# Kernel optimization log

Hardware: AMD Instinct MI355X
Metric: run time of the kernel (lower is better)

## Reference

```python
import jax, jax.numpy as jnp
import numpy as np

B, M, K, N = 4, 2048, 4096, 4096


def setup_inputs() -> dict:
    key = jax.random.key(0)
    k1, k2, k3, k4, k5 = jax.random.split(key, 5)
    # quantized activations in [-8, 7], stored as int8 (spec dtype int32, cast here)
    x_q = jax.random.randint(k1, (B, M, K), -8, 8, dtype=jnp.int32).astype(jnp.int8)
    # per-token activation scales (B, M, 1)
    scales_x = jax.random.uniform(k2, (B, M, 1), dtype=jnp.float32, minval=0.001, maxval=0.02)
    # int8 weight (N, K) in [-8, 7] as produced by from_float
    weight = jax.random.randint(k3, (N, K), -8, 8, dtype=jnp.int32).astype(jnp.int8)
    # per-output-row weight scales (N, 1)
    weight_scales = jax.random.uniform(k4, (N, 1), dtype=jnp.float32, minval=0.001, maxval=0.02)
    bias = jax.random.normal(k5, (N,), dtype=jnp.float32) * 0.02
    return {"x_q": x_q, "scales_x": scales_x, "weight": weight,
            "weight_scales": weight_scales, "bias": bias}


def reference(x_q, scales_x, weight, weight_scales, bias):
    acc = jnp.einsum('bmk,nk->bmn', x_q, weight,
                     preferred_element_type=jnp.int32)  # (B, M, N) int32
    # sym_dequant: per-token scale * per-row weight scale, then fused bias add
    out = acc.astype(jnp.float32) * scales_x * weight_scales.reshape(1, 1, N) + bias
    return out
```

## Files before the change

### kernel.cpp

```cpp
#include <hip/hip_runtime.h>
#include <stdint.h>

#define MROWS 8192
#define K_DIM 4096
#define N_DIM 4096
#define BM 256
#define BN 256
#define BK 64
#define KT (K_DIM / BK)
#define ABYTES (BM * BK)
#define TBYTES (2 * ABYTES)

#define X_ELEMS (MROWS * K_DIM)
#define W_ELEMS (N_DIM * K_DIM)

typedef __attribute__((ext_vector_type(4))) int   int4v;
typedef __attribute__((ext_vector_type(4))) float float4v;

#define GLOAD_LDS16(gptr, lptr)                                                   \
    __builtin_amdgcn_global_load_lds((const __attribute__((address_space(1))) void*)(gptr), \
                                     (__attribute__((address_space(3))) void*)(lptr), 16, 0, 0)

__device__ __forceinline__ int pack4(int4v v) {
    return (int)((unsigned)(v[0] & 0xFF)
               | ((unsigned)(v[1] & 0xFF) << 8)
               | ((unsigned)(v[2] & 0xFF) << 16)
               | ((unsigned)(v[3] & 0xFF) << 24));
}

__global__ __launch_bounds__(256) void pack_i32_to_i8(
    const int4v* __restrict__ src, int* __restrict__ dst, int n4)
{
    int i = blockIdx.x * blockDim.x + threadIdx.x;
    if (i < n4) dst[i] = pack4(src[i]);
}

__global__ __launch_bounds__(512, 2) void i8gemm_dq_kernel(
    const int8_t* __restrict__ xq,
    const float*  __restrict__ sx,
    const int8_t* __restrict__ wt,
    const float*  __restrict__ ws,
    const float*  __restrict__ bias,
    float*        __restrict__ out)
{
    __shared__ __align__(16) int8_t lds8[4 * TBYTES];

    const int tid  = threadIdx.x;
    const int wave = tid >> 6;
    const int lane = tid & 63;
    const int wr   = wave >> 2;
    const int wcn  = wave & 3;

    const int bid = blockIdx.x;
    const int wg  = (bid & 7) * 64 + (bid >> 3);
    const int ct  = wg & 15;
    const int rt  = wg >> 4;

    const int srow = wave * 16 + (lane >> 2);
    const int scol = (((lane & 3) - ((lane >> 3) & 3)) & 3) * 16;
    const int8_t* gA0 = xq + (size_t)(rt * BM + srow) * K_DIM + scol;
    const int8_t* gA1 = gA0 + (size_t)128 * K_DIM;
    const int8_t* gB0 = wt + (size_t)(ct * BN + srow) * K_DIM + scol;
    const int8_t* gB1 = gB0 + (size_t)128 * K_DIM;
    const int dA0 = wave * 1024;
    const int dA1 = 8192 + wave * 1024;
    const int dB0 = ABYTES + wave * 1024;
    const int dB1 = ABYTES + 8192 + wave * 1024;

    const int mrow = lane & 15;
    const int kswz = (((lane >> 4) + (mrow >> 1)) & 3) * 16;
    const int aoff = (wr * 128 + mrow) * BK + kswz;
    const int boff = ABYTES + (wcn * 64 + mrow) * BK + kswz;

    int4v acc[8][4] = {};

    #pragma unroll
    for (int u = 0; u < 3; ++u) {
        const size_t ko = (size_t)u * BK;
        int8_t* bb = lds8 + u * TBYTES;
        GLOAD_LDS16(gA0 + ko, bb + dA0);
        GLOAD_LDS16(gA1 + ko, bb + dA1);
        GLOAD_LDS16(gB0 + ko, bb + dB0);
        GLOAD_LDS16(gB1 + ko, bb + dB1);
    }

    #pragma unroll 4
    for (int t = 0; t < KT; ++t) {
        const int  buf = t & 3;
        const int  nb  = (t + 3) & 3;
        const int  u   = (t + 3) & (KT - 1);
        const size_t ko = (size_t)u * BK;
        const int8_t* base = lds8 + buf * TBYTES;
        int8_t* nbb = lds8 + nb * TBYTES;

        asm volatile("s_waitcnt vmcnt(8)" ::: "memory");
        __builtin_amdgcn_s_barrier();
        __builtin_amdgcn_sched_barrier(0);

        int4v a[4], b[4];
        #pragma unroll
        for (int i = 0; i < 4; ++i) a[i] = *(const int4v*)(base + aoff + i * 1024);
        #pragma unroll
        for (int j = 0; j < 4; ++j) b[j] = *(const int4v*)(base + boff + j * 1024);
        GLOAD_LDS16(gA0 + ko, nbb + dA0);
        GLOAD_LDS16(gA1 + ko, nbb + dA1);

        __builtin_amdgcn_s_setprio(1);
        #pragma unroll
        for (int i = 0; i < 4; ++i)
            #pragma unroll
            for (int j = 0; j < 4; ++j)
                acc[i][j] = __builtin_amdgcn_mfma_i32_16x16x64_i8(a[i], b[j], acc[i][j], 0, 0, 0);
        __builtin_amdgcn_s_setprio(0);

        int4v a2[4];
        #pragma unroll
        for (int i = 0; i < 4; ++i) a2[i] = *(const int4v*)(base + aoff + (4 + i) * 1024);
        GLOAD_LDS16(gB0 + ko, nbb + dB0);
        GLOAD_LDS16(gB1 + ko, nbb + dB1);

        __builtin_amdgcn_s_setprio(1);
        #pragma unroll
        for (int i = 0; i < 4; ++i)
            #pragma unroll
            for (int j = 0; j < 4; ++j)
                acc[4 + i][j] = __builtin_amdgcn_mfma_i32_16x16x64_i8(a2[i], b[j], acc[4 + i][j], 0, 0, 0);
        __builtin_amdgcn_s_setprio(0);
    }

    asm volatile("s_waitcnt vmcnt(0)" ::: "memory");

    const int row_base = rt * BM + wr * 128;
    const int col_base = ct * BN + wcn * 64;
    const int crow = (lane >> 4) * 4;
    const int ccol = lane & 15;

    float wsc[4], bsc[4];
    #pragma unroll
    for (int j = 0; j < 4; ++j) {
        const int c = col_base + j * 16 + ccol;
        wsc[j] = ws[c];
        bsc[j] = bias[c];
    }

    #pragma unroll
    for (int i = 0; i < 8; ++i) {
        const int r0 = row_base + i * 16 + crow;
        const float4v sx4 = *(const float4v*)(sx + r0);
        #pragma unroll
        for (int j = 0; j < 4; ++j) {
            const int c = col_base + j * 16 + ccol;
            float* o = out + (size_t)r0 * N_DIM + c;
            #pragma unroll
            for (int r = 0; r < 4; ++r)
                o[(size_t)r * N_DIM] = (float)acc[i][j][r] * sx4[r] * wsc[j] + bsc[j];
        }
    }
}

extern "C" void kernel_launch(void* const* d_in, const int* in_sizes, int n_in,
                              void* d_out, int out_size, void* d_ws, size_t ws_size,
                              hipStream_t stream) {
    const int*   xq32 = (const int*)d_in[0];
    const float* sx   = (const float*)d_in[1];
    const int*   wt32 = (const int*)d_in[2];
    const float* ws   = (const float*)d_in[3];
    const float* bias = (const float*)d_in[4];
    float* out = (float*)d_out;

    int8_t* xq8 = (int8_t*)d_ws;
    int8_t* wt8 = xq8 + (size_t)X_ELEMS;

    {
        int n4x = X_ELEMS / 4;
        int n4w = W_ELEMS / 4;
        pack_i32_to_i8<<<n4x / 256, 256, 0, stream>>>((const int4v*)xq32, (int*)xq8, n4x);
        pack_i32_to_i8<<<n4w / 256, 256, 0, stream>>>((const int4v*)wt32, (int*)wt8, n4w);
    }

    dim3 grid((MROWS / BM) * (N_DIM / BN));
    i8gemm_dq_kernel<<<grid, 512, 0, stream>>>(xq8, sx, wt8, ws, bias, out);
}
```

Before: 388.5 us.

## Register double-buffer LDS fragments across K tiles and merge pack kernels

```diff
diff --git a/kernel.cpp b/kernel.cpp
--- a/kernel.cpp
+++ b/kernel.cpp
@@ -29,11 +29,44 @@
 }
 
 __global__ __launch_bounds__(256) void pack_i32_to_i8(
-    const int4v* __restrict__ src, int* __restrict__ dst, int n4)
+    const int4v* __restrict__ srcX, int* __restrict__ dstX, int n4x,
+    const int4v* __restrict__ srcW, int* __restrict__ dstW, int n4w)
 {
-    int i = blockIdx.x * blockDim.x + threadIdx.x;
-    if (i < n4) dst[i] = pack4(src[i]);
+    const int stride = gridDim.x * blockDim.x;
+    const int n4 = n4x + n4w;
+    for (int i = blockIdx.x * blockDim.x + threadIdx.x; i < n4; i += stride) {
+        if (i < n4x) dstX[i] = pack4(srcX[i]);
+        else         dstW[i - n4x] = pack4(srcW[i - n4x]);
+    }
 }
+
+
+#define TILE_BODY(T, AC, BC, AN, BN_)                                          \
+  {                                                                            \
+    asm volatile("s_waitcnt vmcnt(4)" ::: "memory");                           \
+    __builtin_amdgcn_s_barrier();                                              \
+    __builtin_amdgcn_sched_barrier(0);                                         \
+    const int u_ = ((T) + 3) & (KT - 1);                                       \
+    const size_t ko_ = (size_t)u_ * BK;                                        \
+    int8_t* nbb_ = lds8 + (((T) + 3) & 3) * TBYTES;                            \
+    GLOAD_LDS16(gA0 + ko_, nbb_ + dA0);                                        \
+    GLOAD_LDS16(gA1 + ko_, nbb_ + dA1);                                        \
+    GLOAD_LDS16(gB0 + ko_, nbb_ + dB0);                                        \
+    GLOAD_LDS16(gB1 + ko_, nbb_ + dB1);                                        \
+    const int8_t* rb_ = lds8 + (((T) + 1) & 3) * TBYTES;                       \
+    _Pragma("unroll") for (int i_ = 0; i_ < 8; ++i_)                           \
+        AN[i_] = *(const int4v*)(rb_ + aoff + i_ * 1024);                      \
+    _Pragma("unroll") for (int j_ = 0; j_ < 4; ++j_)                           \
+        BN_[j_] = *(const int4v*)(rb_ + boff + j_ * 1024);                     \
+    __builtin_amdgcn_sched_barrier(0);                                         \
+    __builtin_amdgcn_s_setprio(1);                                             \
+    _Pragma("unroll") for (int i_ = 0; i_ < 8; ++i_)                           \
+      _Pragma("unroll") for (int j_ = 0; j_ < 4; ++j_)                         \
+        acc[i_][j_] = __builtin_amdgcn_mfma_i32_16x16x64_i8(                   \
+                          AC[i_], BC[j_], acc[i_][j_], 0, 0, 0);               \
+    __builtin_amdgcn_s_setprio(0);                                             \
+    __builtin_amdgcn_sched_barrier(0);                                         \
+  }
 
 __global__ __launch_bounds__(512, 2) void i8gemm_dq_kernel(
     const int8_t* __restrict__ xq,
@@ -84,48 +117,21 @@
         GLOAD_LDS16(gB1 + ko, bb + dB1);
     }
 
-    #pragma unroll 4
-    for (int t = 0; t < KT; ++t) {
-        const int  buf = t & 3;
-        const int  nb  = (t + 3) & 3;
-        const int  u   = (t + 3) & (KT - 1);
-        const size_t ko = (size_t)u * BK;
-        const int8_t* base = lds8 + buf * TBYTES;
-        int8_t* nbb = lds8 + nb * TBYTES;
-
+    int4v a0f[8], b0f[4], a1f[8], b1f[4];
+    {
         asm volatile("s_waitcnt vmcnt(8)" ::: "memory");
         __builtin_amdgcn_s_barrier();
         __builtin_amdgcn_sched_barrier(0);
+        const int8_t* rb = lds8;
+        #pragma unroll
+        for (int i = 0; i < 8; ++i) a0f[i] = *(const int4v*)(rb + aoff + i * 1024);
+        #pragma unroll
+        for (int j = 0; j < 4; ++j) b0f[j] = *(const int4v*)(rb + boff + j * 1024);
+    }
 
-        int4v a[4], b[4];
-        #pragma unroll
-        for (int i = 0; i < 4; ++i) a[i] = *(const int4v*)(base + aoff + i * 1024);
-        #pragma unroll
-        for (int j = 0; j < 4; ++j) b[j] = *(const int4v*)(base + boff + j * 1024);
-        GLOAD_LDS16(gA0 + ko, nbb + dA0);
-        GLOAD_LDS16(gA1 + ko, nbb + dA1);
-
-        __builtin_amdgcn_s_setprio(1);
-        #pragma unroll
-        for (int i = 0; i < 4; ++i)
-            #pragma unroll
-            for (int j = 0; j < 4; ++j)
-                acc[i][j] = __builtin_amdgcn_mfma_i32_16x16x64_i8(a[i], b[j], acc[i][j], 0, 0, 0);
-        __builtin_amdgcn_s_setprio(0);
-
-        int4v a2[4];
-        #pragma unroll
-        for (int i = 0; i < 4; ++i) a2[i] = *(const int4v*)(base + aoff + (4 + i) * 1024);
-        GLOAD_LDS16(gB0 + ko, nbb + dB0);
-        GLOAD_LDS16(gB1 + ko, nbb + dB1);
-
-        __builtin_amdgcn_s_setprio(1);
-        #pragma unroll
-        for (int i = 0; i < 4; ++i)
-            #pragma unroll
-            for (int j = 0; j < 4; ++j)
-                acc[4 + i][j] = __builtin_amdgcn_mfma_i32_16x16x64_i8(a2[i], b[j], acc[4 + i][j], 0, 0, 0);
-        __builtin_amdgcn_s_setprio(0);
+    for (int tt = 0; tt < KT; tt += 2) {
+        TILE_BODY(tt,     a0f, b0f, a1f, b1f);
+        TILE_BODY(tt + 1, a1f, b1f, a0f, b0f);
     }
 
     asm volatile("s_waitcnt vmcnt(0)" ::: "memory");
@@ -174,8 +180,8 @@
     {
         int n4x = X_ELEMS / 4;
         int n4w = W_ELEMS / 4;
-        pack_i32_to_i8<<<n4x / 256, 256, 0, stream>>>((const int4v*)xq32, (int*)xq8, n4x);
-        pack_i32_to_i8<<<n4w / 256, 256, 0, stream>>>((const int4v*)wt32, (int*)wt8, n4w);
+        pack_i32_to_i8<<<2048, 256, 0, stream>>>((const int4v*)xq32, (int*)xq8, n4x,
+                                                 (const int4v*)wt32, (int*)wt8, n4w);
     }
 
     dim3 grid((MROWS / BM) * (N_DIM / BN));
```

Result: no change. 392.7 us (+1.1%).

## Switch GEMM to 32x32x32 int8 MFMA tiles and merge pack kernels

Applied to the files above, without the earlier changes.

```diff
diff --git a/kernel.cpp b/kernel.cpp
--- a/kernel.cpp
+++ b/kernel.cpp
@@ -14,8 +14,9 @@
 #define X_ELEMS (MROWS * K_DIM)
 #define W_ELEMS (N_DIM * K_DIM)
 
-typedef __attribute__((ext_vector_type(4))) int   int4v;
-typedef __attribute__((ext_vector_type(4))) float float4v;
+typedef __attribute__((ext_vector_type(4)))  int   int4v;
+typedef __attribute__((ext_vector_type(16))) int   int16v;
+typedef __attribute__((ext_vector_type(4)))  float float4v;
 
 #define GLOAD_LDS16(gptr, lptr)                                                   \
     __builtin_amdgcn_global_load_lds((const __attribute__((address_space(1))) void*)(gptr), \
@@ -29,10 +30,15 @@
 }
 
 __global__ __launch_bounds__(256) void pack_i32_to_i8(
-    const int4v* __restrict__ src, int* __restrict__ dst, int n4)
+    const int4v* __restrict__ srcX, int* __restrict__ dstX, int n4x,
+    const int4v* __restrict__ srcW, int* __restrict__ dstW, int n4w)
 {
-    int i = blockIdx.x * blockDim.x + threadIdx.x;
-    if (i < n4) dst[i] = pack4(src[i]);
+    const int stride = gridDim.x * blockDim.x;
+    const int n4 = n4x + n4w;
+    for (int i = blockIdx.x * blockDim.x + threadIdx.x; i < n4; i += stride) {
+        if (i < n4x) dstX[i] = pack4(srcX[i]);
+        else         dstW[i - n4x] = pack4(srcW[i - n4x]);
+    }
 }
 
 __global__ __launch_bounds__(512, 2) void i8gemm_dq_kernel(
@@ -67,12 +73,13 @@
     const int dB0 = ABYTES + wave * 1024;
     const int dB1 = ABYTES + 8192 + wave * 1024;
 
-    const int mrow = lane & 15;
-    const int kswz = (((lane >> 4) + (mrow >> 1)) & 3) * 16;
-    const int aoff = (wr * 128 + mrow) * BK + kswz;
-    const int boff = ABYTES + (wcn * 64 + mrow) * BK + kswz;
-
-    int4v acc[8][4] = {};
+    const int m32 = lane & 31;
+    const int hi  = lane >> 5;
+    const int askew = ((hi + (m32 >> 1)) & 3) * 16;
+    const int aoff  = (wr * 128 + m32) * BK;
+    const int boff  = ABYTES + (wcn * 64 + m32) * BK;
+
+    int16v acc[4][2] = {};
 
     #pragma unroll
     for (int u = 0; u < 3; ++u) {
@@ -97,34 +104,49 @@
         __builtin_amdgcn_s_barrier();
         __builtin_amdgcn_sched_barrier(0);
 
-        int4v a[4], b[4];
-        #pragma unroll
-        for (int i = 0; i < 4; ++i) a[i] = *(const int4v*)(base + aoff + i * 1024);
-        #pragma unroll
-        for (int j = 0; j < 4; ++j) b[j] = *(const int4v*)(base + boff + j * 1024);
+        int4v a0[2][2], bf[2][2];
+        #pragma unroll
+        for (int i = 0; i < 2; ++i)
+            #pragma unroll
+            for (int s = 0; s < 2; ++s)
+                a0[i][s] = *(const int4v*)(base + aoff + i * 2048 + (askew ^ (s << 5)));
+        #pragma unroll
+        for (int j = 0; j < 2; ++j)
+            #pragma unroll
+            for (int s = 0; s < 2; ++s)
+                bf[j][s] = *(const int4v*)(base + boff + j * 2048 + (askew ^ (s << 5)));
         GLOAD_LDS16(gA0 + ko, nbb + dA0);
         GLOAD_LDS16(gA1 + ko, nbb + dA1);
 
         __builtin_amdgcn_s_setprio(1);
         #pragma unroll
-        for (int i = 0; i < 4; ++i)
-            #pragma unroll
-            for (int j = 0; j < 4; ++j)
-                acc[i][j] = __builtin_amdgcn_mfma_i32_16x16x64_i8(a[i], b[j], acc[i][j], 0, 0, 0);
+        for (int s = 0; s < 2; ++s)
+            #pragma unroll
+            for (int i = 0; i < 2; ++i)
+                #pragma unroll
+                for (int j = 0; j < 2; ++j)
+                    acc[i][j] = __builtin_amdgcn_mfma_i32_32x32x32_i8(
+                                    a0[i][s], bf[j][s], acc[i][j], 0, 0, 0);
         __builtin_amdgcn_s_setprio(0);
 
-        int4v a2[4];
-        #pragma unroll
-        for (int i = 0; i < 4; ++i) a2[i] = *(const int4v*)(base + aoff + (4 + i) * 1024);
+        int4v a1[2][2];
+        #pragma unroll
+        for (int i = 0; i < 2; ++i)
+            #pragma unroll
+            for (int s = 0; s < 2; ++s)
+                a1[i][s] = *(const int4v*)(base + aoff + (2 + i) * 2048 + (askew ^ (s << 5)));
         GLOAD_LDS16(gB0 + ko, nbb + dB0);
         GLOAD_LDS16(gB1 + ko, nbb + dB1);
 
         __builtin_amdgcn_s_setprio(1);
         #pragma unroll
-        for (int i = 0; i < 4; ++i)
-            #pragma unroll
-            for (int j = 0; j < 4; ++j)
-                acc[4 + i][j] = __builtin_amdgcn_mfma_i32_16x16x64_i8(a2[i], b[j], acc[4 + i][j], 0, 0, 0);
+        for (int s = 0; s < 2; ++s)
+            #pragma unroll
+            for (int i = 0; i < 2; ++i)
+                #pragma unroll
+                for (int j = 0; j < 2; ++j)
+                    acc[2 + i][j] = __builtin_amdgcn_mfma_i32_32x32x32_i8(
+                                        a1[i][s], bf[j][s], acc[2 + i][j], 0, 0, 0);
         __builtin_amdgcn_s_setprio(0);
     }
 
@@ -132,28 +154,29 @@
 
     const int row_base = rt * BM + wr * 128;
     const int col_base = ct * BN + wcn * 64;
-    const int crow = (lane >> 4) * 4;
-    const int ccol = lane & 15;
-
-    float wsc[4], bsc[4];
+
+    float wsc[2], bsc[2];
     #pragma unroll
-    for (int j = 0; j < 4; ++j) {
-        const int c = col_base + j * 16 + ccol;
+    for (int j = 0; j < 2; ++j) {
+        const int c = col_base + j * 32 + m32;
         wsc[j] = ws[c];
         bsc[j] = bias[c];
     }
 
     #pragma unroll
-    for (int i = 0; i < 8; ++i) {
-        const int r0 = row_base + i * 16 + crow;
-        const float4v sx4 = *(const float4v*)(sx + r0);
-        #pragma unroll
-        for (int j = 0; j < 4; ++j) {
-            const int c = col_base + j * 16 + ccol;
-            float* o = out + (size_t)r0 * N_DIM + c;
-            #pragma unroll
-            for (int r = 0; r < 4; ++r)
-                o[(size_t)r * N_DIM] = (float)acc[i][j][r] * sx4[r] * wsc[j] + bsc[j];
+    for (int i = 0; i < 4; ++i) {
+        #pragma unroll
+        for (int q = 0; q < 4; ++q) {
+            const int r0 = row_base + i * 32 + q * 8 + hi * 4;
+            const float4v sx4 = *(const float4v*)(sx + r0);
+            #pragma unroll
+            for (int j = 0; j < 2; ++j) {
+                const int c = col_base + j * 32 + m32;
+                float* o = out + (size_t)r0 * N_DIM + c;
+                #pragma unroll
+                for (int r = 0; r < 4; ++r)
+                    o[(size_t)r * N_DIM] = (float)acc[i][j][q * 4 + r] * sx4[r] * wsc[j] + bsc[j];
+            }
         }
     }
 }
@@ -174,8 +197,8 @@
     {
         int n4x = X_ELEMS / 4;
         int n4w = W_ELEMS / 4;
-        pack_i32_to_i8<<<n4x / 256, 256, 0, stream>>>((const int4v*)xq32, (int*)xq8, n4x);
-        pack_i32_to_i8<<<n4w / 256, 256, 0, stream>>>((const int4v*)wt32, (int*)wt8, n4w);
+        pack_i32_to_i8<<<2048, 256, 0, stream>>>((const int4v*)xq32, (int*)xq8, n4x,
+                                                 (const int4v*)wt32, (int*)wt8, n4w);
     }
 
     dim3 grid((MROWS / BM) * (N_DIM / BN));
```

After: 404.0 us. +4.0%, slower.

## Merge pack kernels and add ping-pong barriers around MFMA phases

Applied to the files above, without the earlier changes.

```diff
diff --git a/kernel.cpp b/kernel.cpp
--- a/kernel.cpp
+++ b/kernel.cpp
@@ -29,10 +29,15 @@
 }
 
 __global__ __launch_bounds__(256) void pack_i32_to_i8(
-    const int4v* __restrict__ src, int* __restrict__ dst, int n4)
+    const int4v* __restrict__ srcX, int* __restrict__ dstX, int n4x,
+    const int4v* __restrict__ srcW, int* __restrict__ dstW, int n4w)
 {
-    int i = blockIdx.x * blockDim.x + threadIdx.x;
-    if (i < n4) dst[i] = pack4(src[i]);
+    const int stride = gridDim.x * blockDim.x;
+    const int n4 = n4x + n4w;
+    for (int i = blockIdx.x * blockDim.x + threadIdx.x; i < n4; i += stride) {
+        if (i < n4x) dstX[i] = pack4(srcX[i]);
+        else         dstW[i - n4x] = pack4(srcW[i - n4x]);
+    }
 }
 
 __global__ __launch_bounds__(512, 2) void i8gemm_dq_kernel(
@@ -83,19 +88,16 @@
         GLOAD_LDS16(gB0 + ko, bb + dB0);
         GLOAD_LDS16(gB1 + ko, bb + dB1);
     }
+    asm volatile("s_waitcnt vmcnt(8)" ::: "memory");
+    __builtin_amdgcn_s_barrier();
 
     #pragma unroll 4
     for (int t = 0; t < KT; ++t) {
         const int  buf = t & 3;
-        const int  nb  = (t + 3) & 3;
         const int  u   = (t + 3) & (KT - 1);
         const size_t ko = (size_t)u * BK;
         const int8_t* base = lds8 + buf * TBYTES;
-        int8_t* nbb = lds8 + nb * TBYTES;
-
-        asm volatile("s_waitcnt vmcnt(8)" ::: "memory");
-        __builtin_amdgcn_s_barrier();
-        __builtin_amdgcn_sched_barrier(0);
+        int8_t* nbb = lds8 + ((t + 3) & 3) * TBYTES;
 
         int4v a[4], b[4];
         #pragma unroll
@@ -104,28 +106,37 @@
         for (int j = 0; j < 4; ++j) b[j] = *(const int4v*)(base + boff + j * 1024);
         GLOAD_LDS16(gA0 + ko, nbb + dA0);
         GLOAD_LDS16(gA1 + ko, nbb + dA1);
-
+        __builtin_amdgcn_s_barrier();
+        asm volatile("s_waitcnt lgkmcnt(0)" ::: "memory");
+        __builtin_amdgcn_sched_barrier(0);
         __builtin_amdgcn_s_setprio(1);
         #pragma unroll
         for (int i = 0; i < 4; ++i)
             #pragma unroll
             for (int j = 0; j < 4; ++j)
-                acc[i][j] = __builtin_amdgcn_mfma_i32_16x16x64_i8(a[i], b[j], acc[i][j], 0, 0, 0);
+                acc[i][j] = __builtin_amdgcn_mfma_i32_16x16x64_i8(
+                                a[i], b[j], acc[i][j], 0, 0, 0);
         __builtin_amdgcn_s_setprio(0);
+        __builtin_amdgcn_s_barrier();
 
         int4v a2[4];
         #pragma unroll
         for (int i = 0; i < 4; ++i) a2[i] = *(const int4v*)(base + aoff + (4 + i) * 1024);
         GLOAD_LDS16(gB0 + ko, nbb + dB0);
         GLOAD_LDS16(gB1 + ko, nbb + dB1);
-
+        __builtin_amdgcn_s_barrier();
+        asm volatile("s_waitcnt lgkmcnt(0)" ::: "memory");
+        __builtin_amdgcn_sched_barrier(0);
         __builtin_amdgcn_s_setprio(1);
         #pragma unroll
         for (int i = 0; i < 4; ++i)
             #pragma unroll
             for (int j = 0; j < 4; ++j)
-                acc[4 + i][j] = __builtin_amdgcn_mfma_i32_16x16x64_i8(a2[i], b[j], acc[4 + i][j], 0, 0, 0);
+                acc[4 + i][j] = __builtin_amdgcn_mfma_i32_16x16x64_i8(
+                                    a2[i], b[j], acc[4 + i][j], 0, 0, 0);
         __builtin_amdgcn_s_setprio(0);
+        asm volatile("s_waitcnt vmcnt(8)" ::: "memory");
+        __builtin_amdgcn_s_barrier();
     }
 
     asm volatile("s_waitcnt vmcnt(0)" ::: "memory");
@@ -174,8 +185,8 @@
     {
         int n4x = X_ELEMS / 4;
         int n4w = W_ELEMS / 4;
-        pack_i32_to_i8<<<n4x / 256, 256, 0, stream>>>((const int4v*)xq32, (int*)xq8, n4x);
-        pack_i32_to_i8<<<n4w / 256, 256, 0, stream>>>((const int4v*)wt32, (int*)wt8, n4w);
+        pack_i32_to_i8<<<2048, 256, 0, stream>>>((const int4v*)xq32, (int*)xq8, n4x,
+                                                 (const int4v*)wt32, (int*)wt8, n4w);
     }
 
     dim3 grid((MROWS / BM) * (N_DIM / BN));
```

After: 399.7 us. 1.03x slower.
